# Kernel optimization log

Hardware: AMD Instinct MI355X
Metric: run time of the kernel (lower is better)

## Reference

```python
import jax, jax.numpy as jnp
import numpy as np


def setup_inputs() -> dict:
    key = jax.random.key(0)
    ks = jax.random.split(key, 5)
    T, B, E = 2048, 2, 1024
    return {
        "query": jax.random.normal(ks[0], (T, B, E), dtype=jnp.float32),
        "in_proj_weight": jax.random.normal(ks[1], (3 * E, E), dtype=jnp.float32) * (E ** -0.5),
        "in_proj_bias": jax.random.normal(ks[2], (3 * E,), dtype=jnp.float32) * 0.02,
        "out_proj_weight": jax.random.normal(ks[3], (E, E), dtype=jnp.float32) * (E ** -0.5),
        "out_proj_bias": jax.random.normal(ks[4], (E,), dtype=jnp.float32) * 0.02,
        "num_heads": 16,
    }


def reference(query, in_proj_weight, in_proj_bias, out_proj_weight, out_proj_bias, num_heads):
    T, B, E = query.shape
    H = num_heads
    d = E // H
    scaling = d ** -0.5
    # fused QKV projection: (T,B,E) @ (E,3E) + bias -> (T,B,3E)
    qkv = jnp.einsum('tbe,fe->tbf', query, in_proj_weight) + in_proj_bias
    # torch views (T*B, 3E) as (T, B*H, 3, d): per token layout is (H, 3, d)
    qkv = qkv.reshape(T, B, H, 3, d)
    q = qkv[..., 0, :] * scaling  # (T,B,H,d)
    k = qkv[..., 1, :]
    v = qkv[..., 2, :]
    scores = jnp.einsum('tbhd,sbhd->bhts', q, k)  # (B,H,T,T)
    probs = jax.nn.softmax(scores.astype(jnp.float32), axis=-1).astype(scores.dtype)
    ctx = jnp.einsum('bhts,sbhd->tbhd', probs, v).reshape(T, B, E)
    out = jnp.einsum('tbe,fe->tbf', ctx, out_proj_weight) + out_proj_bias
    return out
```

## Files before the change

kernel.cpp:

```cpp
#include <hip/hip_runtime.h>
#include <hip/hip_bf16.h>
#include <math.h>

constexpr int T_DIM = 2048;
constexpr int B_DIM = 2;
constexpr int E_DIM = 1024;
constexpr float QK_SCALE = 0.18033688011112042f;

#if __has_builtin(__builtin_amdgcn_exp2f)
#define EXP2F(x) __builtin_amdgcn_exp2f(x)
#else
#define EXP2F(x) exp2f(x)
#endif

typedef __attribute__((ext_vector_type(8))) short short8;
typedef __attribute__((ext_vector_type(4))) float f32x4;

__device__ inline short f2bf(float x) {
    union { __hip_bfloat16 b; short s; } u;
    u.b = __float2bfloat16(x);
    return u.s;
}
__device__ inline float bf2f(short s) {
    union { __hip_bfloat16 b; short s; } u;
    u.s = s;
    return __bfloat162float(u.b);
}

__device__ inline int pack_bf16(float hi, float lo) {
    union { float f; unsigned u; } a, b;
    a.f = hi; b.f = lo;
    return (int)__builtin_amdgcn_perm(a.u + 0x8000u, b.u + 0x8000u, 0x07060302u);
}

__device__ inline void gl2lds16(const void* g, void* l) {
    __builtin_amdgcn_global_load_lds(
        (const __attribute__((address_space(1))) unsigned int*)g,
        (__attribute__((address_space(3))) unsigned int*)l, 16, 0, 0);
}

__device__ inline f32x4 mfma_bf16(short8 a, short8 b, f32x4 c) {
    return __builtin_amdgcn_mfma_f32_16x16x32_bf16(a, b, c, 0, 0, 0);
}

__global__ __launch_bounds__(256)
void split_all_kernel(const float* __restrict__ query,
                      const float* __restrict__ w_in,
                      const float* __restrict__ w_out,
                      short* __restrict__ qh,
                      short* __restrict__ wih, short* __restrict__ wil,
                      short* __restrict__ woh, short* __restrict__ wol,
                      int nq4, int nwi4, int nwo4)
{
    int i = blockIdx.x * 256 + threadIdx.x;
    const float* src; short* dh; short* dl; int k; int do_lo;
    if (i < nq4) { src = query; dh = qh; dl = nullptr; k = i; do_lo = 0; }
    else if (i < nq4 + nwi4) { src = w_in; dh = wih; dl = wil; k = i - nq4; do_lo = 1; }
    else { src = w_out; dh = woh; dl = wol; k = i - nq4 - nwi4; do_lo = 1; }
    float4 v = ((const float4*)src)[k];
    short h0 = f2bf(v.x), h1 = f2bf(v.y), h2 = f2bf(v.z), h3 = f2bf(v.w);
    ((short4*)dh)[k] = make_short4(h0, h1, h2, h3);
    if (do_lo) {
        short l0 = f2bf(v.x - bf2f(h0));
        short l1 = f2bf(v.y - bf2f(h1));
        short l2 = f2bf(v.z - bf2f(h2));
        short l3 = f2bf(v.w - bf2f(h3));
        ((short4*)dl)[k] = make_short4(l0, l1, l2, l3);
    }
}

__global__ __launch_bounds__(256)
void gemm_in(const short* __restrict__ Ah,
             const short* __restrict__ Wh, const short* __restrict__ Wl,
             const float* __restrict__ bias,
             short* __restrict__ qkv, short* __restrict__ kp,
             short* __restrict__ vtp,
             int M, int N, int K)
{
    __shared__ __align__(16) short AsH[128 * 64];
    __shared__ __align__(16) short WsH[128 * 64];
    __shared__ __align__(16) short WsL[128 * 64];

    const int tid  = threadIdx.x;
    const int lane = tid & 63;
    const int wave = tid >> 6;
    const int rm = (wave >> 1) * 64;
    const int cn = (wave & 1) * 64;
    const int m0 = blockIdx.y * 128;
    const int n0 = blockIdx.x * 128;

    const int srow = wave * 32 + (lane >> 3);
    const int swz  = (lane & 7) ^ (lane >> 3);
    const size_t gaB = (size_t)(m0 + srow) * K + swz * 8;
    const size_t gwB = (size_t)(n0 + srow) * K + swz * 8;
    const size_t rowK8 = (size_t)8 * K;

    const f32x4 zero = {0.f, 0.f, 0.f, 0.f};
    f32x4 acc[4][4];
    #pragma unroll
    for (int i = 0; i < 4; ++i)
        #pragma unroll
        for (int j = 0; j < 4; ++j) acc[i][j] = zero;

    const int fr = lane & 15;
    const int qc = lane >> 4;

    for (int k0 = 0; k0 < K; k0 += 64) {
        if (k0) __syncthreads();
        #pragma unroll
        for (int c = 0; c < 4; ++c) {
            gl2lds16(Ah + gaB + k0 + c * rowK8, &AsH[(wave * 32 + c * 8) * 64]);
            gl2lds16(Wh + gwB + k0 + c * rowK8, &WsH[(wave * 32 + c * 8) * 64]);
            gl2lds16(Wl + gwB + k0 + c * rowK8, &WsL[(wave * 32 + c * 8) * 64]);
        }
        __syncthreads();

        #pragma unroll
        for (int kk = 0; kk < 2; ++kk) {
            short8 ahf[4], bhf[4], blf[4];
            #pragma unroll
            for (int i = 0; i < 4; ++i) {
                int r = rm + 16 * i + fr;
                int slot = (4 * kk + qc) ^ (r & 7);
                ahf[i] = *(const short8*)&AsH[r * 64 + slot * 8];
            }
            #pragma unroll
            for (int j = 0; j < 4; ++j) {
                int r = cn + 16 * j + fr;
                int slot = (4 * kk + qc) ^ (r & 7);
                bhf[j] = *(const short8*)&WsH[r * 64 + slot * 8];
                blf[j] = *(const short8*)&WsL[r * 64 + slot * 8];
            }
            #pragma unroll
            for (int i = 0; i < 4; ++i)
                #pragma unroll
                for (int j = 0; j < 4; ++j) {
                    acc[i][j] = mfma_bf16(ahf[i], bhf[j], acc[i][j]);
                    acc[i][j] = mfma_bf16(ahf[i], blf[j], acc[i][j]);
                }
        }
    }

    const int g = lane >> 4;
    #pragma unroll
    for (int j = 0; j < 4; ++j) {
        const int colu = n0 + cn + 16 * j;
        const int col  = colu + fr;
        const float bj = bias[col];
        const int c6  = colu >> 6;
        const int grp = c6 % 3;
        const int h   = c6 / 3;
        const int d   = (colu & 63) + fr;
        if (grp == 0) {
            #pragma unroll
            for (int i = 0; i < 4; ++i)
                #pragma unroll
                for (int r = 0; r < 4; ++r) {
                    int row = m0 + rm + 16 * i + g * 4 + r;
                    qkv[(size_t)row * 3072 + col] =
                        f2bf((acc[i][j][r] + bj) * QK_SCALE);
                }
        } else if (grp == 1) {
            const int hh = d >> 5, gk = (d >> 3) & 3, ii = d & 7;
            #pragma unroll
            for (int i = 0; i < 4; ++i)
                #pragma unroll
                for (int r = 0; r < 4; ++r) {
                    int row = m0 + rm + 16 * i + g * 4 + r;
                    int t = row >> 1, bb = row & 1;
                    int m = t & 63;
                    int R = (m & 32) | ((m & 24) >> 1) | ((m & 4) << 2) | (m & 3);
                    size_t off = (size_t)(bb * 16 + h) * 131072
                               + (size_t)(t >> 6) * 4096
                               + (size_t)(((2 * (R >> 4) + hh) * 64
                                           + gk * 16 + (R & 15)) * 8 + ii);
                    kp[off] = f2bf(acc[i][j][r] + bj);
                }
        } else {
            const int jd = d >> 4, frv = d & 15;
            #pragma unroll
            for (int i = 0; i < 4; ++i)
                #pragma unroll
                for (int r = 0; r < 4; ++r) {
                    int row = m0 + rm + 16 * i + g * 4 + r;
                    int t = row >> 1, bb = row & 1;
                    int tl = t & 63;
                    size_t off = (size_t)(bb * 16 + h) * 131072
                               + (size_t)(t >> 6) * 4096
                               + (size_t)(((2 * jd + (tl >> 5)) * 64
                                           + ((tl >> 3) & 3) * 16 + frv) * 8
                                          + (tl & 7));
                    vtp[off] = f2bf(acc[i][j][r] + bj);
                }
        }
    }
}

__global__ __launch_bounds__(256)
void gemm_out(const short* __restrict__ Ah, const short* __restrict__ Al,
              const short* __restrict__ Wh, const short* __restrict__ Wl,
              const float* __restrict__ bias, float* __restrict__ Cout,
              int M, int N, int K)
{
    __shared__ __align__(16) short AsH[64 * 64];
    __shared__ __align__(16) short AsL[64 * 64];
    __shared__ __align__(16) short WsH[128 * 64];
    __shared__ __align__(16) short WsL[128 * 64];

    const int tid  = threadIdx.x;
    const int lane = tid & 63;
    const int wave = tid >> 6;
    const int m0 = blockIdx.y * 64;
    const int n0 = blockIdx.x * 128;

    const int sarow = wave * 16 + (lane >> 3);
    const int swrow = wave * 32 + (lane >> 3);
    const int swz   = (lane & 7) ^ (lane >> 3);
    const size_t gaB = (size_t)(m0 + sarow) * K + swz * 8;
    const size_t gwB = (size_t)(n0 + swrow) * K + swz * 8;
    const size_t rowK8 = (size_t)8 * K;

    const f32x4 zero = {0.f, 0.f, 0.f, 0.f};
    f32x4 acc[4][2];
    #pragma unroll
    for (int i = 0; i < 4; ++i) { acc[i][0] = zero; acc[i][1] = zero; }

    const int fr = lane & 15;
    const int g = lane >> 4;

    for (int k0 = 0; k0 < K; k0 += 64) {
        if (k0) __syncthreads();
        #pragma unroll
        for (int c = 0; c < 2; ++c) {
            gl2lds16(Ah + gaB + k0 + c * rowK8, &AsH[(wave * 16 + c * 8) * 64]);
            gl2lds16(Al + gaB + k0 + c * rowK8, &AsL[(wave * 16 + c * 8) * 64]);
        }
        #pragma unroll
        for (int c = 0; c < 4; ++c) {
            gl2lds16(Wh + gwB + k0 + c * rowK8, &WsH[(wave * 32 + c * 8) * 64]);
            gl2lds16(Wl + gwB + k0 + c * rowK8, &WsL[(wave * 32 + c * 8) * 64]);
        }
        __syncthreads();

        #pragma unroll
        for (int kk = 0; kk < 2; ++kk) {
            short8 ahf[4], alf[4], bhf[2], blf[2];
            #pragma unroll
            for (int i = 0; i < 4; ++i) {
                int r = 16 * i + fr;
                int slot = (4 * kk + g) ^ (r & 7);
                ahf[i] = *(const short8*)&AsH[r * 64 + slot * 8];
                alf[i] = *(const short8*)&AsL[r * 64 + slot * 8];
            }
            #pragma unroll
            for (int j = 0; j < 2; ++j) {
                int r = wave * 32 + 16 * j + fr;
                int slot = (4 * kk + g) ^ (r & 7);
                bhf[j] = *(const short8*)&WsH[r * 64 + slot * 8];
                blf[j] = *(const short8*)&WsL[r * 64 + slot * 8];
            }
            #pragma unroll
            for (int i = 0; i < 4; ++i)
                #pragma unroll
                for (int j = 0; j < 2; ++j) {
                    acc[i][j] = mfma_bf16(ahf[i], bhf[j], acc[i][j]);
                    acc[i][j] = mfma_bf16(ahf[i], blf[j], acc[i][j]);
                    acc[i][j] = mfma_bf16(alf[i], bhf[j], acc[i][j]);
                }
        }
    }

    #pragma unroll
    for (int j = 0; j < 2; ++j) {
        int col = n0 + wave * 32 + 16 * j + fr;
        float bj = bias[col];
        #pragma unroll
        for (int i = 0; i < 4; ++i)
            #pragma unroll
            for (int r = 0; r < 4; ++r) {
                int row = m0 + 16 * i + g * 4 + r;
                Cout[(size_t)row * N + col] = acc[i][j][r] + bj;
            }
    }
}

__global__ __launch_bounds__(256, 2)
void attn_mfma(const short* __restrict__ qkv, const short* __restrict__ kp,
               const short* __restrict__ vtp,
               short* __restrict__ ctxh, short* __restrict__ ctxl)
{
    __shared__ __align__(16) short ldsK[2][4096];
    __shared__ __align__(16) short ldsV[2][4096];

    const int tid  = threadIdx.x;
    const int lane = tid & 63;
    const int wave = tid >> 6;
    const int fr = lane & 15;
    const int g  = lane >> 4;

    const int id = blockIdx.x;
    const int x = id & 7, y = id >> 3;
    const int bh = x * 4 + (y & 3);
    const int q0 = (y >> 2) * 128;
    const int b = bh >> 4, h = bh & 15;

    short8 aq[2][2];
    #pragma unroll
    for (int set = 0; set < 2; ++set) {
        const short* qrow = qkv +
            ((size_t)(q0 + wave * 32 + set * 16 + fr) * 2 + b) * 3072 + h * 192;
        aq[set][0] = *(const short8*)(qrow + g * 8);
        aq[set][1] = *(const short8*)(qrow + 32 + g * 8);
    }

    const short* kt = kp  + (size_t)bh * 131072;
    const short* vt = vtp + (size_t)bh * 131072;

    short8 ONES;
    #pragma unroll
    for (int i = 0; i < 8; ++i) ONES[i] = (short)0x3F80;

    const f32x4 zero = {0.f, 0.f, 0.f, 0.f};
    f32x4 o[2][4];
    #pragma unroll
    for (int set = 0; set < 2; ++set)
        #pragma unroll
        for (int jd = 0; jd < 4; ++jd) o[set][jd] = zero;
    f32x4 lacc[2] = {zero, zero};

    auto stage = [&](int it, int sel) {
        const short* ks = kt + it * 4096 + wave * 1024 + lane * 8;
        const short* vs = vt + it * 4096 + wave * 1024 + lane * 8;
        gl2lds16(ks,       &ldsK[sel][wave * 1024]);
        gl2lds16(ks + 512, &ldsK[sel][wave * 1024 + 512]);
        gl2lds16(vs,       &ldsV[sel][wave * 1024]);
        gl2lds16(vs + 512, &ldsV[sel][wave * 1024 + 512]);
    };

    stage(0, 0);
    #pragma unroll 2
    for (int it = 0; it < 32; ++it) {
        const int cur = it & 1;
        __syncthreads();
        if (it + 1 < 32) stage(it + 1, cur ^ 1);

        int afw[2][2][4];
        #pragma unroll
        for (int s = 0; s < 4; ++s) {
            short8 k0 = *(const short8*)&ldsK[cur][(2 * s) * 512 + lane * 8];
            short8 k1 = *(const short8*)&ldsK[cur][(2 * s + 1) * 512 + lane * 8];
            #pragma unroll
            for (int set = 0; set < 2; ++set) {
                f32x4 a = zero;
                a = mfma_bf16(k0, aq[set][0], a);
                a = mfma_bf16(k1, aq[set][1], a);
                float e0 = EXP2F(a[0]), e1 = EXP2F(a[1]);
                float e2 = EXP2F(a[2]), e3 = EXP2F(a[3]);
                afw[set][s >> 1][(s & 1) * 2]     = pack_bf16(e1, e0);
                afw[set][s >> 1][(s & 1) * 2 + 1] = pack_bf16(e3, e2);
            }
        }
        union { int w[4]; short8 v; } A[2][2];
        #pragma unroll
        for (int set = 0; set < 2; ++set)
            #pragma unroll
            for (int hh = 0; hh < 2; ++hh)
                #pragma unroll
                for (int w = 0; w < 4; ++w) A[set][hh].w[w] = afw[set][hh][w];

        #pragma unroll
        for (int set = 0; set < 2; ++set) {
            lacc[set] = mfma_bf16(A[set][0].v, ONES, lacc[set]);
            lacc[set] = mfma_bf16(A[set][1].v, ONES, lacc[set]);
        }

        #pragma unroll
        for (int jd = 0; jd < 4; ++jd) {
            short8 v0 = *(const short8*)&ldsV[cur][(2 * jd) * 512 + lane * 8];
            short8 v1 = *(const short8*)&ldsV[cur][(2 * jd + 1) * 512 + lane * 8];
            #pragma unroll
            for (int set = 0; set < 2; ++set) {
                o[set][jd] = mfma_bf16(A[set][0].v, v0, o[set][jd]);
                o[set][jd] = mfma_bf16(A[set][1].v, v1, o[set][jd]);
            }
        }
    }

    #pragma unroll
    for (int set = 0; set < 2; ++set)
        #pragma unroll
        for (int r = 0; r < 4; ++r) {
            float inv = 1.f / lacc[set][r];
            int t = q0 + wave * 32 + set * 16 + 4 * g + r;
            size_t base = ((size_t)t * B_DIM + b) * E_DIM + h * 64;
            #pragma unroll
            for (int jd = 0; jd < 4; ++jd) {
                float v = o[set][jd][r] * inv;
                short hs = f2bf(v);
                short ls = f2bf(v - bf2f(hs));
                ctxh[base + 16 * jd + fr] = hs;
                ctxl[base + 16 * jd + fr] = ls;
            }
        }
}

extern "C" void kernel_launch(void* const* d_in, const int* in_sizes, int n_in,
                              void* d_out, int out_size, void* d_ws, size_t ws_size,
                              hipStream_t stream)
{
    const float* query = (const float*)d_in[0];
    const float* w_in  = (const float*)d_in[1];
    const float* b_in  = (const float*)d_in[2];
    const float* w_out = (const float*)d_in[3];
    const float* b_out = (const float*)d_in[4];
    float* out = (float*)d_out;

    char* ws = (char*)d_ws;
    short* qkv  = (short*)(ws);
    short* qh   = (short*)(ws + 25165824);
    short* wih  = (short*)(ws + 33554432);
    short* wil  = (short*)(ws + 39845888);
    short* woh  = (short*)(ws + 46137344);
    short* wol  = (short*)(ws + 48234496);
    short* vtp  = (short*)(ws + 50331648);
    short* kp   = (short*)(ws + 58720256);
    short* ctxh = (short*)(ws + 25165824);
    short* ctxl = (short*)(ws + 33554432);

    const int M = T_DIM * B_DIM;

    int nq4  = (M * E_DIM) / 4;
    int nwi4 = (3 * E_DIM * E_DIM) / 4;
    int nwo4 = (E_DIM * E_DIM) / 4;
    split_all_kernel<<<(nq4 + nwi4 + nwo4) / 256, 256, 0, stream>>>(
        query, w_in, w_out, qh, wih, wil, woh, wol, nq4, nwi4, nwo4);

    gemm_in<<<dim3(3 * E_DIM / 128, M / 128), 256, 0, stream>>>(
        qh, wih, wil, b_in, qkv, kp, vtp, M, 3 * E_DIM, E_DIM);

    attn_mfma<<<dim3(512), 256, 0, stream>>>(qkv, kp, vtp, ctxh, ctxl);

    gemm_out<<<dim3(E_DIM / 128, M / 64), 256, 0, stream>>>(
        ctxh, ctxl, woh, wol, b_out, out, M, E_DIM, E_DIM);
}
```

Measured before the change: 208.4 us.

## Split attention key range across two wave groups and reduce partials in LDS

```diff
diff --git a/kernel.cpp b/kernel.cpp
--- a/kernel.cpp
+++ b/kernel.cpp
@@ -284,17 +284,18 @@
     }
 }
 
-__global__ __launch_bounds__(256, 2)
+__global__ __launch_bounds__(512, 4)
 void attn_mfma(const short* __restrict__ qkv, const short* __restrict__ kp,
                const short* __restrict__ vtp,
                short* __restrict__ ctxh, short* __restrict__ ctxl)
 {
-    __shared__ __align__(16) short ldsK[2][4096];
-    __shared__ __align__(16) short ldsV[2][4096];
+    __shared__ __align__(16) short ldsKV[2][2][8192];
 
     const int tid  = threadIdx.x;
     const int lane = tid & 63;
     const int wave = tid >> 6;
+    const int w4    = wave & 3;
+    const int khalf = wave >> 2;
     const int fr = lane & 15;
     const int g  = lane >> 4;
 
@@ -308,13 +309,13 @@
     #pragma unroll
     for (int set = 0; set < 2; ++set) {
         const short* qrow = qkv +
-            ((size_t)(q0 + wave * 32 + set * 16 + fr) * 2 + b) * 3072 + h * 192;
+            ((size_t)(q0 + w4 * 32 + set * 16 + fr) * 2 + b) * 3072 + h * 192;
         aq[set][0] = *(const short8*)(qrow + g * 8);
         aq[set][1] = *(const short8*)(qrow + 32 + g * 8);
     }
 
-    const short* kt = kp  + (size_t)bh * 131072;
-    const short* vt = vtp + (size_t)bh * 131072;
+    const short* kt = kp  + (size_t)bh * 131072 + (size_t)khalf * 16 * 4096;
+    const short* vt = vtp + (size_t)bh * 131072 + (size_t)khalf * 16 * 4096;
 
     short8 ONES;
     #pragma unroll
@@ -329,26 +330,29 @@
     f32x4 lacc[2] = {zero, zero};
 
     auto stage = [&](int it, int sel) {
-        const short* ks = kt + it * 4096 + wave * 1024 + lane * 8;
-        const short* vs = vt + it * 4096 + wave * 1024 + lane * 8;
-        gl2lds16(ks,       &ldsK[sel][wave * 1024]);
-        gl2lds16(ks + 512, &ldsK[sel][wave * 1024 + 512]);
-        gl2lds16(vs,       &ldsV[sel][wave * 1024]);
-        gl2lds16(vs + 512, &ldsV[sel][wave * 1024 + 512]);
+        const short* ks = kt + it * 4096 + w4 * 1024 + lane * 8;
+        const short* vs = vt + it * 4096 + w4 * 1024 + lane * 8;
+        short* base = &ldsKV[khalf][sel][0];
+        gl2lds16(ks,       base + w4 * 1024);
+        gl2lds16(ks + 512, base + w4 * 1024 + 512);
+        gl2lds16(vs,       base + 4096 + w4 * 1024);
+        gl2lds16(vs + 512, base + 4096 + w4 * 1024 + 512);
     };
 
     stage(0, 0);
     #pragma unroll 2
-    for (int it = 0; it < 32; ++it) {
+    for (int it = 0; it < 16; ++it) {
         const int cur = it & 1;
         __syncthreads();
-        if (it + 1 < 32) stage(it + 1, cur ^ 1);
-
-        int afw[2][2][4];
-        #pragma unroll
-        for (int s = 0; s < 4; ++s) {
-            short8 k0 = *(const short8*)&ldsK[cur][(2 * s) * 512 + lane * 8];
-            short8 k1 = *(const short8*)&ldsK[cur][(2 * s + 1) * 512 + lane * 8];
+        if (it + 1 < 16) stage(it + 1, cur ^ 1);
+        const short* Kb = &ldsKV[khalf][cur][0];
+        const short* Vb = Kb + 4096;
+
+        union { int w[4]; short8 v; } A0[2];
+        #pragma unroll
+        for (int s = 0; s < 2; ++s) {
+            short8 k0 = *(const short8*)&Kb[(2 * s) * 512 + lane * 8];
+            short8 k1 = *(const short8*)&Kb[(2 * s + 1) * 512 + lane * 8];
             #pragma unroll
             for (int set = 0; set < 2; ++set) {
                 f32x4 a = zero;
@@ -356,52 +360,86 @@
                 a = mfma_bf16(k1, aq[set][1], a);
                 float e0 = EXP2F(a[0]), e1 = EXP2F(a[1]);
                 float e2 = EXP2F(a[2]), e3 = EXP2F(a[3]);
-                afw[set][s >> 1][(s & 1) * 2]     = pack_bf16(e1, e0);
-                afw[set][s >> 1][(s & 1) * 2 + 1] = pack_bf16(e3, e2);
-            }
-        }
-        union { int w[4]; short8 v; } A[2][2];
+                A0[set].w[s * 2]     = pack_bf16(e1, e0);
+                A0[set].w[s * 2 + 1] = pack_bf16(e3, e2);
+            }
+        }
         #pragma unroll
         for (int set = 0; set < 2; ++set)
-            #pragma unroll
-            for (int hh = 0; hh < 2; ++hh)
-                #pragma unroll
-                for (int w = 0; w < 4; ++w) A[set][hh].w[w] = afw[set][hh][w];
-
-        #pragma unroll
-        for (int set = 0; set < 2; ++set) {
-            lacc[set] = mfma_bf16(A[set][0].v, ONES, lacc[set]);
-            lacc[set] = mfma_bf16(A[set][1].v, ONES, lacc[set]);
-        }
-
+            lacc[set] = mfma_bf16(A0[set].v, ONES, lacc[set]);
         #pragma unroll
         for (int jd = 0; jd < 4; ++jd) {
-            short8 v0 = *(const short8*)&ldsV[cur][(2 * jd) * 512 + lane * 8];
-            short8 v1 = *(const short8*)&ldsV[cur][(2 * jd + 1) * 512 + lane * 8];
+            short8 v0 = *(const short8*)&Vb[(2 * jd) * 512 + lane * 8];
+            #pragma unroll
+            for (int set = 0; set < 2; ++set)
+                o[set][jd] = mfma_bf16(A0[set].v, v0, o[set][jd]);
+        }
+
+        union { int w[4]; short8 v; } A1[2];
+        #pragma unroll
+        for (int s = 0; s < 2; ++s) {
+            short8 k0 = *(const short8*)&Kb[(2 * s + 4) * 512 + lane * 8];
+            short8 k1 = *(const short8*)&Kb[(2 * s + 5) * 512 + lane * 8];
             #pragma unroll
             for (int set = 0; set < 2; ++set) {
-                o[set][jd] = mfma_bf16(A[set][0].v, v0, o[set][jd]);
-                o[set][jd] = mfma_bf16(A[set][1].v, v1, o[set][jd]);
-            }
-        }
-    }
-
-    #pragma unroll
-    for (int set = 0; set < 2; ++set)
-        #pragma unroll
-        for (int r = 0; r < 4; ++r) {
-            float inv = 1.f / lacc[set][r];
-            int t = q0 + wave * 32 + set * 16 + 4 * g + r;
-            size_t base = ((size_t)t * B_DIM + b) * E_DIM + h * 64;
-            #pragma unroll
-            for (int jd = 0; jd < 4; ++jd) {
-                float v = o[set][jd][r] * inv;
-                short hs = f2bf(v);
-                short ls = f2bf(v - bf2f(hs));
-                ctxh[base + 16 * jd + fr] = hs;
-                ctxl[base + 16 * jd + fr] = ls;
-            }
-        }
+                f32x4 a = zero;
+                a = mfma_bf16(k0, aq[set][0], a);
+                a = mfma_bf16(k1, aq[set][1], a);
+                float e0 = EXP2F(a[0]), e1 = EXP2F(a[1]);
+                float e2 = EXP2F(a[2]), e3 = EXP2F(a[3]);
+                A1[set].w[s * 2]     = pack_bf16(e1, e0);
+                A1[set].w[s * 2 + 1] = pack_bf16(e3, e2);
+            }
+        }
+        #pragma unroll
+        for (int set = 0; set < 2; ++set)
+            lacc[set] = mfma_bf16(A1[set].v, ONES, lacc[set]);
+        #pragma unroll
+        for (int jd = 0; jd < 4; ++jd) {
+            short8 v1 = *(const short8*)&Vb[(2 * jd + 1) * 512 + lane * 8];
+            #pragma unroll
+            for (int set = 0; set < 2; ++set)
+                o[set][jd] = mfma_bf16(A1[set].v, v1, o[set][jd]);
+        }
+    }
+
+    __syncthreads();
+    float* oshare = (float*)&ldsKV[0][0][0];
+    float* lshare = oshare + 128 * 68;
+
+    if (khalf == 1) {
+        #pragma unroll
+        for (int set = 0; set < 2; ++set)
+            #pragma unroll
+            for (int r = 0; r < 4; ++r) {
+                int row = w4 * 32 + set * 16 + 4 * g + r;
+                #pragma unroll
+                for (int jd = 0; jd < 4; ++jd)
+                    oshare[row * 68 + 16 * jd + fr] = o[set][jd][r];
+                if (fr == 0) lshare[row] = lacc[set][r];
+            }
+    }
+    __syncthreads();
+    if (khalf == 0) {
+        #pragma unroll
+        for (int set = 0; set < 2; ++set)
+            #pragma unroll
+            for (int r = 0; r < 4; ++r) {
+                int row = w4 * 32 + set * 16 + 4 * g + r;
+                float lt = lacc[set][r] + lshare[row];
+                float inv = 1.f / lt;
+                int t = q0 + row;
+                size_t base = ((size_t)t * B_DIM + b) * E_DIM + h * 64;
+                #pragma unroll
+                for (int jd = 0; jd < 4; ++jd) {
+                    float v = (o[set][jd][r] + oshare[row * 68 + 16 * jd + fr]) * inv;
+                    short hs = f2bf(v);
+                    short ls = f2bf(v - bf2f(hs));
+                    ctxh[base + 16 * jd + fr] = hs;
+                    ctxl[base + 16 * jd + fr] = ls;
+                }
+            }
+    }
 }
 
 extern "C" void kernel_launch(void* const* d_in, const int* in_sizes, int n_in,
@@ -438,7 +476,7 @@
     gemm_in<<<dim3(3 * E_DIM / 128, M / 128), 256, 0, stream>>>(
         qh, wih, wil, b_in, qkv, kp, vtp, M, 3 * E_DIM, E_DIM);
 
-    attn_mfma<<<dim3(512), 256, 0, stream>>>(qkv, kp, vtp, ctxh, ctxl);
+    attn_mfma<<<dim3(512), 512, 0, stream>>>(qkv, kp, vtp, ctxh, ctxl);
 
     gemm_out<<<dim3(E_DIM / 128, M / 64), 256, 0, stream>>>(
         ctxh, ctxl, woh, wol, b_out, out, M, E_DIM, E_DIM);
```

Result: faster. 197.0 us (median of 2 runs) (-5.5%).
